# Kernel tuning notes

Measured on AMD Instinct MI355X. Metric: run time of the kernel, lower is better.

The kernel has to match this reference:

```python
import jax, jax.numpy as jnp
import numpy as np

B, U1, U2 = 4, 2048, 2048
C = 256      # in_feat_dim
F = 256      # feat_dim
M = 4        # num_modes
D = C // M   # attention_mode_dim = 64
ATTN_CLIP = 500.0
LN_EPS = 1e-12


def setup_inputs() -> dict:
    key = jax.random.key(0)
    ks = jax.random.split(key, 8)
    s = 0.02  # base_initializer_range
    inp = {
        "query_feat": jax.random.normal(ks[0], (B, U1, C), jnp.float32),
        "key_feat": jax.random.normal(ks[1], (B, U2, C), jnp.float32),
        "Wq": jax.random.normal(ks[2], (M * D, C), jnp.float32) * s,
        "bq": jnp.zeros((M * D,), jnp.float32),
    }
    # tie_qk_scheme='shared': key linear shares query weights
    inp["Wk"] = inp["Wq"]
    inp["bk"] = inp["bq"]
    inp["Wv"] = jax.random.normal(ks[3], (M * F, C), jnp.float32) * s  # first_linear, v_has_bias=False
    inp["W_mid"] = jax.random.normal(ks[4], (F, F), jnp.float32) * s   # MMSharedMid shared_linear
    inp["b_mid"] = jnp.zeros((F,), jnp.float32)
    inp["W_out"] = jax.random.normal(ks[5], (M, F, F), jnp.float32) * s  # grouped 1x1 conv, per mode
    inp["b_out"] = jnp.zeros((M, F), jnp.float32)
    inp["ln_g"] = jnp.ones((F,), jnp.float32)   # resout LayerNorm
    inp["ln_b"] = jnp.zeros((F,), jnp.float32)
    inp["W_score"] = jax.random.normal(ks[6], (1, F), jnp.float32) * s  # LearnedSoftAggregate
    inp["b_score"] = jnp.zeros((1,), jnp.float32)
    return inp


def _layer_norm(x, g, b):
    mu = jnp.mean(x, axis=-1, keepdims=True)
    var = jnp.var(x, axis=-1, keepdims=True)
    return (x - mu) * jax.lax.rsqrt(var + LN_EPS) * g + b


def reference(query_feat, key_feat, Wq, bq, Wk, bk, Wv, W_mid, b_mid,
              W_out, b_out, ln_g, ln_b, W_score, b_score):
    # --- tied-QK multi-mode attention ---
    q = (query_feat @ Wq.T + bq).reshape(B, U1, M, D)
    k = (key_feat @ Wk.T + bk).reshape(B, U2, M, D)
    scores = jnp.einsum('bimd,bjmd->bmij', q, k) / jnp.sqrt(jnp.float32(D))
    scores = jnp.clip(scores, -ATTN_CLIP, ATTN_CLIP)  # attn_clip
    probs = jax.nn.softmax(scores, axis=-1)           # [B, M, U1, U2]

    # --- ExpandedFeatTrans: value projection + fusion ---
    v = (key_feat @ Wv.T).reshape(B, U2, M, F)        # first_linear (no bias)
    fused = jnp.einsum('bmij,bjmf->bmif', probs, v)   # [B, M, U1, F]

    # MMSharedMid: shared linear over F + gelu (dropout = identity in eval)
    mid = jax.nn.gelu(fused @ W_mid.T + b_mid, approximate=False)

    # MMPrivateOutput: per-mode grouped 1x1 conv; NOTE the original code computes
    # x_comb = x + shortcut but then layer-norms x (shortcut dropped) - kept faithful.
    out = jnp.einsum('bmif,mgf->bmig', mid, W_out) + b_out[None, :, None, :]
    out = _layer_norm(out, ln_g, ln_b)                # [B, M, U1, F]

    # LearnedSoftAggregate over modes (group_dim=1, keepdim=False)
    mode_scores = out @ W_score.T + b_score           # [B, M, U1, 1]
    mode_probs = jax.nn.softmax(mode_scores, axis=1)
    return jnp.sum(out * mode_probs, axis=1)          # [B, U1, F]
```

## Files before the change

### kernel.cpp

```cpp
#include <hip/hip_runtime.h>

typedef __attribute__((ext_vector_type(8))) short short8;
typedef __attribute__((ext_vector_type(4))) float f32x4;
typedef __attribute__((ext_vector_type(16))) float f32x16;
typedef unsigned short u16t;
typedef unsigned int u32t;

#define MFMA16(a, b, c) __builtin_amdgcn_mfma_f32_16x16x32_bf16((a), (b), (c), 0, 0, 0)
#define MFMA32(a, b, c) __builtin_amdgcn_mfma_f32_32x32x16_bf16((a), (b), (c), 0, 0, 0)

__device__ __forceinline__ u16t f2bf(float f) {
  u32t u = __float_as_uint(f);
  u32t r = u + 0x7fffu + ((u >> 16) & 1u);
  return (u16t)(r >> 16);
}
__device__ __forceinline__ float bf2f(u16t b) {
  return __uint_as_float(((u32t)b) << 16);
}
__device__ __forceinline__ short8 pack8(float4 a0, float4 a1) {
  short8 r;
  r[0] = (short)f2bf(a0.x); r[1] = (short)f2bf(a0.y);
  r[2] = (short)f2bf(a0.z); r[3] = (short)f2bf(a0.w);
  r[4] = (short)f2bf(a1.x); r[5] = (short)f2bf(a1.y);
  r[6] = (short)f2bf(a1.z); r[7] = (short)f2bf(a1.w);
  return r;
}
__device__ __forceinline__ u32t packrhu(float a, float b) {
  u32t ua = __float_as_uint(a) + 0x8000u;
  u32t ub = __float_as_uint(b) + 0x8000u;
  return (ua >> 16) | (ub & 0xffff0000u);
}

__device__ __forceinline__ void proj_dev(
    const float* __restrict__ A, const float* __restrict__ W,
    const float* __restrict__ bias, float scale,
    u16t* __restrict__ out, int mode, int bx, int by,
    u16t* As, u16t* Ws) {
  const int tid = threadIdx.x;
  const int w = tid >> 6, lane = tid & 63, quad = lane >> 4, l15 = lane & 15;
  const int l31 = lane & 31, h8 = (lane >> 5) * 8;
  const int rt = bx * 64;
  const int ct = by * 64;
  const int wrow = (w >> 1) * 32, wcol = (w & 1) * 32;
  const int r2 = tid >> 3, c8 = tid & 7;

  const f32x4 fzero = {0.f, 0.f, 0.f, 0.f};
  f32x4 acc[2][2];
#pragma unroll
  for (int i = 0; i < 2; i++)
#pragma unroll
    for (int j = 0; j < 2; j++) acc[i][j] = fzero;

  for (int kt = 0; kt < 4; ++kt) {
    __syncthreads();
#pragma unroll
    for (int hh = 0; hh < 2; ++hh) {
      int rr = r2 + hh * 32;
      const float4* pa = (const float4*)(A + (size_t)(rt + rr) * 256 + kt * 64 + c8 * 8);
      const float4* pw = (const float4*)(W + (size_t)(ct + rr) * 256 + kt * 64 + c8 * 8);
      float4 w0 = pw[0], w1 = pw[1];
      w0.x *= scale; w0.y *= scale; w0.z *= scale; w0.w *= scale;
      w1.x *= scale; w1.y *= scale; w1.z *= scale; w1.w *= scale;
      *(short8*)&As[rr * 72 + c8 * 8] = pack8(pa[0], pa[1]);
      *(short8*)&Ws[rr * 72 + c8 * 8] = pack8(w0, w1);
    }
    __syncthreads();
#pragma unroll
    for (int ks = 0; ks < 2; ++ks) {
      short8 af0 = *(const short8*)&As[(wrow + l15) * 72 + ks * 32 + quad * 8];
      short8 af1 = *(const short8*)&As[(wrow + 16 + l15) * 72 + ks * 32 + quad * 8];
      short8 bw0 = *(const short8*)&Ws[(wcol + l15) * 72 + ks * 32 + quad * 8];
      short8 bw1 = *(const short8*)&Ws[(wcol + 16 + l15) * 72 + ks * 32 + quad * 8];
      acc[0][0] = MFMA16(af0, bw0, acc[0][0]);
      acc[0][1] = MFMA16(af0, bw1, acc[0][1]);
      acc[1][0] = MFMA16(af1, bw0, acc[1][0]);
      acc[1][1] = MFMA16(af1, bw1, acc[1][1]);
    }
  }

  __syncthreads();
  u16t* Cs = As;
  if (mode == 0) {
#pragma unroll
    for (int i = 0; i < 2; i++) {
      int rl = wrow + i * 16 + quad * 4;
#pragma unroll
      for (int j = 0; j < 2; j++) {
        int cl = wcol + j * 16 + l15;
        float bv = bias ? bias[ct + cl] * scale : 0.f;
#pragma unroll
        for (int rg = 0; rg < 4; ++rg)
          Cs[(rl + rg) * 72 + cl] = f2bf(acc[i][j][rg] + bv);
      }
    }
  } else {
#pragma unroll
    for (int i = 0; i < 2; i++) {
      int rl = wrow + i * 16 + quad * 4;
#pragma unroll
      for (int j = 0; j < 2; j++) {
        int cl = wcol + j * 16 + l15;
        ushort4 pk;
        pk.x = f2bf(acc[i][j][0]);
        pk.y = f2bf(acc[i][j][1]);
        pk.z = f2bf(acc[i][j][2]);
        pk.w = f2bf(acc[i][j][3]);
        *(ushort4*)&Cs[cl * 72 + rl] = pk;
      }
    }
  }
  __syncthreads();

#pragma unroll
  for (int t2 = 0; t2 < 2; ++t2) {
    short8 frag = *(const short8*)&Cs[(t2 * 32 + l31) * 72 + w * 16 + h8];
    size_t base;
    if (mode == 0) {
      int b = rt >> 11, m = by;
      int it32 = ((rt & 2047) >> 5) + t2;
      base = (((size_t)(b * 4 + m) * 64 + it32) * 4 + w) * 512;
    } else {
      int b = rt >> 11, m = by >> 2;
      int fb = ((by & 3) << 1) + t2;
      int jt16 = ((rt & 2047) >> 4) + w;
      base = (((size_t)(b * 4 + m) * 8 + fb) * 128 + jt16) * 512;
    }
    *(short8*)(out + base + lane * 8) = frag;
  }
}

__global__ __launch_bounds__(256) void prep_kernel(
    const float* __restrict__ query, const float* __restrict__ key,
    const float* __restrict__ Wq, const float* __restrict__ bq,
    const float* __restrict__ Wv, const float* __restrict__ Wm,
    const float* __restrict__ Wo,
    u16t* __restrict__ WmB, u16t* __restrict__ WoB,
    u16t* __restrict__ QfB, u16t* __restrict__ KfB, u16t* __restrict__ VfB) {
  __shared__ __align__(16) u16t As[64 * 72];
  __shared__ __align__(16) u16t Ws[64 * 72];
  const int blk = blockIdx.x;
  const int tid = threadIdx.x;
  if (blk < 256) {
    int i = blk * 256 + tid;
    WmB[i] = f2bf(Wm[i]);
    return;
  }
  if (blk < 1280) {
    int i = (blk - 256) * 256 + tid;
    WoB[i] = f2bf(Wo[i]);
    return;
  }
  const float *A, *W, *bias;
  float scale;
  u16t* out;
  int mode, local;
  if (blk < 1792) {
    local = blk - 1280; A = query; W = Wq; bias = bq; scale = 0.125f; out = QfB; mode = 0;
  } else if (blk < 2304) {
    local = blk - 1792; A = key; W = Wq; bias = bq; scale = 1.0f; out = KfB; mode = 0;
  } else {
    local = blk - 2304; A = key; W = Wv; bias = nullptr; scale = 1.0f; out = VfB; mode = 1;
  }
  proj_dev(A, W, bias, scale, out, mode, local & 127, local >> 7, As, Ws);
}

__global__ __launch_bounds__(512, 4) void attn_kernel(
    const u16t* __restrict__ Qf, const u16t* __restrict__ Kf,
    const u16t* __restrict__ Vf,
    const u16t* __restrict__ Wmid, const u16t* __restrict__ Wout,
    const float* __restrict__ b_mid, const float* __restrict__ b_out,
    const float* __restrict__ ln_g, const float* __restrict__ ln_b,
    const float* __restrict__ Wsc, const float* __restrict__ b_sc,
    u16t* __restrict__ out_ln, float* __restrict__ scoresWS) {
  __shared__ __align__(16) u16t smF[64 * 264];
  __shared__ __align__(16) u16t smP[2][64 * 132];
  __shared__ float smL[256];
  __shared__ float smR[256];
  __shared__ float smS[128];
  const int tid = threadIdx.x;
  const int w = tid >> 6, lane = tid & 63, quad = lane >> 4, l15 = lane & 15;
  const int l31 = lane & 31, h = lane >> 5;
  const int L = blockIdx.x;
  const int xcd = L & 7, slot = L >> 3;
  const int bm = xcd * 2 + (slot >> 5);
  const int it64 = slot & 31;
  const int m = bm & 3;
  const int q0 = it64 * 64;
  const int jw = w & 3, ihS = w >> 2;

  const size_t lane8 = (size_t)lane * 8;

  const u16t* qbase = Qf + ((size_t)(bm * 64 + it64 * 2 + ihS) * 4) * 512 + lane8;
  short8 qf4[4];
#pragma unroll
  for (int ksd = 0; ksd < 4; ++ksd)
    qf4[ksd] = *(const short8*)(qbase + ksd * 512);

  const u16t* kbase = Kf + ((size_t)bm * 256) * 512 + lane8;
  const u16t* vbase = Vf + ((size_t)(bm * 8 + w) * 128) * 512 + lane8;

  f32x16 facc[2];
#pragma unroll
  for (int j = 0; j < 2; j++)
#pragma unroll
    for (int r = 0; r < 16; r++) facc[j][r] = 0.f;
  float lsum = 0.f;

  short8 kf4[4];
#pragma unroll
  for (int ksd = 0; ksd < 4; ++ksd)
    kf4[ksd] = *(const short8*)(kbase + (size_t)jw * 2048 + ksd * 512);

  {
    f32x16 sacc;
#pragma unroll
    for (int r = 0; r < 16; r++) sacc[r] = 0.f;
#pragma unroll
    for (int ksd = 0; ksd < 4; ++ksd)
      sacc = MFMA32(kf4[ksd], qf4[ksd], sacc);
    float ls = 0.f;
#pragma unroll
    for (int tt = 0; tt < 8; ++tt) {
      const int jl = ((2 * tt) & 3) + 8 * ((2 * tt) >> 2) + 4 * h;
      float p0 = __expf(sacc[2 * tt]);
      float p1 = __expf(sacc[2 * tt + 1]);
      ls += p0 + p1;
      *(u32t*)&smP[0][(ihS * 32 + l31) * 132 + jw * 32 + jl] = packrhu(p0, p1);
    }
    lsum += ls;
  }
#pragma unroll
  for (int ksd = 0; ksd < 4; ++ksd)
    kf4[ksd] = *(const short8*)(kbase + (size_t)(4 + jw) * 2048 + ksd * 512);
  __syncthreads();

#pragma unroll 1
  for (int t = 0; t < 16; ++t) {
    u16t* Pb = &smP[t & 1][0];
    u16t* Pn = &smP[(t + 1) & 1][0];

    if (t < 15) {
      f32x16 sacc;
#pragma unroll
      for (int r = 0; r < 16; r++) sacc[r] = 0.f;
#pragma unroll
      for (int ksd = 0; ksd < 4; ++ksd)
        sacc = MFMA32(kf4[ksd], qf4[ksd], sacc);
      float ls = 0.f;
#pragma unroll
      for (int tt = 0; tt < 8; ++tt) {
        const int jl = ((2 * tt) & 3) + 8 * ((2 * tt) >> 2) + 4 * h;
        float p0 = __expf(sacc[2 * tt]);
        float p1 = __expf(sacc[2 * tt + 1]);
        ls += p0 + p1;
        *(u32t*)&Pn[(ihS * 32 + l31) * 132 + jw * 32 + jl] = packrhu(p0, p1);
      }
      lsum += ls;
    }
    if (t < 14) {
      const int jn = (t + 2) * 4 + jw;
#pragma unroll
      for (int ksd = 0; ksd < 4; ++ksd)
        kf4[ksd] = *(const short8*)(kbase + (size_t)jn * 2048 + ksd * 512);
    }
#pragma unroll
    for (int ks = 0; ks < 8; ++ks) {
      short8 vf = *(const short8*)(vbase + ((size_t)(t * 8 + ks)) * 512);
      short8 b0 = *(const short8*)&Pb[l31 * 132 + ks * 16 + h * 8];
      short8 b1 = *(const short8*)&Pb[(32 + l31) * 132 + ks * 16 + h * 8];
      facc[0] = MFMA32(vf, b0, facc[0]);
      facc[1] = MFMA32(vf, b1, facc[1]);
    }
    __syncthreads();
  }

  lsum += __shfl_xor(lsum, 32);
  if (h == 0) smL[w * 32 + l31] = lsum;
  __syncthreads();
  float inv[2];
#pragma unroll
  for (int ih = 0; ih < 2; ++ih)
    inv[ih] = 1.f / (smL[(ih * 4 + 0) * 32 + l31] + smL[(ih * 4 + 1) * 32 + l31] +
                     smL[(ih * 4 + 2) * 32 + l31] + smL[(ih * 4 + 3) * 32 + l31]);

#pragma unroll
  for (int ih = 0; ih < 2; ++ih) {
#pragma unroll
    for (int g = 0; g < 4; ++g) {
      int fbase = w * 32 + 8 * g + 4 * h;
      ushort4 pk4;
      pk4.x = f2bf(facc[ih][4 * g + 0] * inv[ih]);
      pk4.y = f2bf(facc[ih][4 * g + 1] * inv[ih]);
      pk4.z = f2bf(facc[ih][4 * g + 2] * inv[ih]);
      pk4.w = f2bf(facc[ih][4 * g + 3] * inv[ih]);
      *(ushort4*)&smF[(ih * 32 + l31) * 264 + fbase] = pk4;
    }
  }
  __syncthreads();

  const int rgrp = w >> 1, ch = w & 1;
  const int rowq = rgrp * 16 + quad * 4;
  const f32x4 fz4 = {0.f, 0.f, 0.f, 0.f};

  f32x4 macc[8];
#pragma unroll
  for (int i = 0; i < 8; i++) macc[i] = fz4;
  for (int kc = 0; kc < 8; ++kc) {
    short8 af = *(const short8*)&smF[(rgrp * 16 + l15) * 264 + kc * 32 + quad * 8];
#pragma unroll
    for (int nb = 0; nb < 8; ++nb) {
      short8 bw = *(const short8*)(Wmid + (size_t)(ch * 128 + nb * 16 + l15) * 256 + kc * 32 + quad * 8);
      macc[nb] = MFMA16(af, bw, macc[nb]);
    }
  }
#pragma unroll
  for (int nb = 0; nb < 8; ++nb) {
    int c = ch * 128 + nb * 16 + l15;
    float bmv = b_mid[c];
#pragma unroll
    for (int rg = 0; rg < 4; ++rg) {
      float x = macc[nb][rg] + bmv;
      macc[nb][rg] = 0.5f * x * (1.f + erff(x * 0.70710678118654752f));
    }
  }
  __syncthreads();
#pragma unroll
  for (int nb = 0; nb < 8; ++nb)
#pragma unroll
    for (int rg = 0; rg < 4; ++rg)
      smF[(rowq + rg) * 264 + ch * 128 + nb * 16 + l15] = f2bf(macc[nb][rg]);
  __syncthreads();

  const u16t* Wo = Wout + (size_t)m * 65536;
  f32x4 oacc[8];
#pragma unroll
  for (int i = 0; i < 8; i++) oacc[i] = fz4;
  for (int kc = 0; kc < 8; ++kc) {
    short8 af = *(const short8*)&smF[(rgrp * 16 + l15) * 264 + kc * 32 + quad * 8];
#pragma unroll
    for (int nb = 0; nb < 8; ++nb) {
      short8 bw = *(const short8*)(Wo + (size_t)(ch * 128 + nb * 16 + l15) * 256 + kc * 32 + quad * 8);
      oacc[nb] = MFMA16(af, bw, oacc[nb]);
    }
  }

  float sum[4] = {0, 0, 0, 0}, sq[4] = {0, 0, 0, 0};
#pragma unroll
  for (int nb = 0; nb < 8; ++nb) {
    int c = ch * 128 + nb * 16 + l15;
    float bo = b_out[m * 256 + c];
#pragma unroll
    for (int rg = 0; rg < 4; ++rg) {
      float x = oacc[nb][rg] + bo;
      oacc[nb][rg] = x;
      sum[rg] += x;
      sq[rg] += x * x;
    }
  }
#pragma unroll
  for (int rg = 0; rg < 4; ++rg) {
    float s = sum[rg], s2 = sq[rg];
    s += __shfl_xor(s, 1); s += __shfl_xor(s, 2); s += __shfl_xor(s, 4); s += __shfl_xor(s, 8);
    s2 += __shfl_xor(s2, 1); s2 += __shfl_xor(s2, 2); s2 += __shfl_xor(s2, 4); s2 += __shfl_xor(s2, 8);
    if (l15 == 0) {
      smR[(rowq + rg) + 64 * ch] = s;
      smR[128 + (rowq + rg) + 64 * ch] = s2;
    }
  }
  __syncthreads();
  float mu[4], rstd[4];
#pragma unroll
  for (int rg = 0; rg < 4; ++rg) {
    int r = rowq + rg;
    float s = smR[r] + smR[r + 64];
    float s2 = smR[128 + r] + smR[128 + r + 64];
    float mean = s * (1.f / 256.f);
    float var = s2 * (1.f / 256.f) - mean * mean;
    mu[rg] = mean;
    rstd[rg] = rsqrtf(var + 1e-12f);
  }

  float scp[4] = {0, 0, 0, 0};
#pragma unroll
  for (int nb = 0; nb < 8; ++nb) {
    int c = ch * 128 + nb * 16 + l15;
    float g = ln_g[c], bb2 = ln_b[c], wsv = Wsc[c];
#pragma unroll
    for (int rg = 0; rg < 4; ++rg) {
      float xn = (oacc[nb][rg] - mu[rg]) * rstd[rg] * g + bb2;
      out_ln[((size_t)bm * 2048 + (q0 + rowq + rg)) * 256 + c] = f2bf(xn);
      scp[rg] += xn * wsv;
    }
  }
#pragma unroll
  for (int rg = 0; rg < 4; ++rg) {
    float s = scp[rg];
    s += __shfl_xor(s, 1); s += __shfl_xor(s, 2); s += __shfl_xor(s, 4); s += __shfl_xor(s, 8);
    if (l15 == 0) smS[(rowq + rg) + 64 * ch] = s;
  }
  __syncthreads();
  if (ch == 0 && l15 == 0) {
#pragma unroll
    for (int rg = 0; rg < 4; ++rg) {
      int r = rowq + rg;
      scoresWS[bm * 2048 + q0 + r] = smS[r] + smS[r + 64] + b_sc[0];
    }
  }
}

__global__ __launch_bounds__(256) void agg_kernel(
    const u16t* __restrict__ out_ln, const float* __restrict__ scoresWS,
    float* __restrict__ out) {
  const int row = blockIdx.x;
  const int c = threadIdx.x;
  const int b = row >> 11, i = row & 2047;
  float s0 = scoresWS[(b * 4 + 0) * 2048 + i];
  float s1 = scoresWS[(b * 4 + 1) * 2048 + i];
  float s2 = scoresWS[(b * 4 + 2) * 2048 + i];
  float s3 = scoresWS[(b * 4 + 3) * 2048 + i];
  float mx = fmaxf(fmaxf(s0, s1), fmaxf(s2, s3));
  float e0 = __expf(s0 - mx), e1 = __expf(s1 - mx), e2 = __expf(s2 - mx), e3 = __expf(s3 - mx);
  float inv = 1.f / (e0 + e1 + e2 + e3);
  float acc = e0 * inv * bf2f(out_ln[((size_t)(b * 4 + 0) * 2048 + i) * 256 + c]) +
              e1 * inv * bf2f(out_ln[((size_t)(b * 4 + 1) * 2048 + i) * 256 + c]) +
              e2 * inv * bf2f(out_ln[((size_t)(b * 4 + 2) * 2048 + i) * 256 + c]) +
              e3 * inv * bf2f(out_ln[((size_t)(b * 4 + 3) * 2048 + i) * 256 + c]);
  out[(size_t)row * 256 + c] = acc;
}

extern "C" void kernel_launch(void* const* d_in, const int* in_sizes, int n_in,
                              void* d_out, int out_size, void* d_ws, size_t ws_size,
                              hipStream_t stream) {
  (void)in_sizes; (void)n_in; (void)out_size; (void)ws_size;
  const float* query = (const float*)d_in[0];
  const float* key   = (const float*)d_in[1];
  const float* Wq    = (const float*)d_in[2];
  const float* bq    = (const float*)d_in[3];
  const float* Wv    = (const float*)d_in[6];
  const float* Wm    = (const float*)d_in[7];
  const float* bmid  = (const float*)d_in[8];
  const float* Wo    = (const float*)d_in[9];
  const float* bo    = (const float*)d_in[10];
  const float* lng   = (const float*)d_in[11];
  const float* lnb   = (const float*)d_in[12];
  const float* Wsc   = (const float*)d_in[13];
  const float* bsc   = (const float*)d_in[14];

  char* p = (char*)d_ws;
  u16t* QfB = (u16t*)p; p += (size_t)2097152 * 2;
  u16t* KfB = (u16t*)p; p += (size_t)2097152 * 2;
  u16t* VfB = (u16t*)p; p += (size_t)8388608 * 2;
  u16t* WmB = (u16t*)p; p += (size_t)65536 * 2;
  u16t* WoB = (u16t*)p; p += (size_t)262144 * 2;
  u16t* outLn = (u16t*)p; p += (size_t)8388608 * 2;
  float* scWS = (float*)p; p += (size_t)32768 * 4;

  prep_kernel<<<4352, 256, 0, stream>>>(query, key, Wq, bq, Wv, Wm, Wo,
                                        WmB, WoB, QfB, KfB, VfB);

  attn_kernel<<<512, 512, 0, stream>>>(QfB, KfB, VfB, WmB, WoB,
                                       bmid, bo, lng, lnb, Wsc, bsc,
                                       outLn, scWS);

  agg_kernel<<<8192, 256, 0, stream>>>(outLn, scWS, (float*)d_out);
}
```

Before: 281.8 us.

## Halve attention query tile to 32 rows, doubling blocks and occupancy

Each attention block now handles 32 query rows instead of 64. All 8 waves split the key dimension (8 key tiles per step, 8 steps) and each holds one accumulator. The probability buffer and the fused-feature buffer share one LDS allocation, launch bounds ask for 8 blocks per CU, and the grid doubles to 1024 blocks. This should raise occupancy and cut the tail effect, at the cost of reading each V and K tile twice as often in total and paying more per-block overhead in the MLP/LN epilogue.

```diff
diff --git a/kernel.cpp b/kernel.cpp
--- a/kernel.cpp
+++ b/kernel.cpp
@@ -164,7 +164,7 @@
   proj_dev(A, W, bias, scale, out, mode, local & 127, local >> 7, As, Ws);
 }
 
-__global__ __launch_bounds__(512, 4) void attn_kernel(
+__global__ __launch_bounds__(512, 8) void attn_kernel(
     const u16t* __restrict__ Qf, const u16t* __restrict__ Kf,
     const u16t* __restrict__ Vf,
     const u16t* __restrict__ Wmid, const u16t* __restrict__ Wout,
@@ -172,8 +172,7 @@
     const float* __restrict__ ln_g, const float* __restrict__ ln_b,
     const float* __restrict__ Wsc, const float* __restrict__ b_sc,
     u16t* __restrict__ out_ln, float* __restrict__ scoresWS) {
-  __shared__ __align__(16) u16t smF[64 * 264];
-  __shared__ __align__(16) u16t smP[2][64 * 132];
+  __shared__ __align__(16) u16t smU[16640];
   __shared__ float smL[256];
   __shared__ float smR[256];
   __shared__ float smS[128];
@@ -182,15 +181,14 @@
   const int l31 = lane & 31, h = lane >> 5;
   const int L = blockIdx.x;
   const int xcd = L & 7, slot = L >> 3;
-  const int bm = xcd * 2 + (slot >> 5);
-  const int it64 = slot & 31;
+  const int bm = xcd * 2 + (slot >> 6);
+  const int it32 = slot & 63;
   const int m = bm & 3;
-  const int q0 = it64 * 64;
-  const int jw = w & 3, ihS = w >> 2;
+  const int q0 = it32 * 32;
 
   const size_t lane8 = (size_t)lane * 8;
 
-  const u16t* qbase = Qf + ((size_t)(bm * 64 + it64 * 2 + ihS) * 4) * 512 + lane8;
+  const u16t* qbase = Qf + ((size_t)(bm * 64 + it32) * 4) * 512 + lane8;
   short8 qf4[4];
 #pragma unroll
   for (int ksd = 0; ksd < 4; ++ksd)
@@ -199,17 +197,15 @@
   const u16t* kbase = Kf + ((size_t)bm * 256) * 512 + lane8;
   const u16t* vbase = Vf + ((size_t)(bm * 8 + w) * 128) * 512 + lane8;
 
-  f32x16 facc[2];
-#pragma unroll
-  for (int j = 0; j < 2; j++)
-#pragma unroll
-    for (int r = 0; r < 16; r++) facc[j][r] = 0.f;
+  f32x16 facc;
+#pragma unroll
+  for (int r = 0; r < 16; r++) facc[r] = 0.f;
   float lsum = 0.f;
 
   short8 kf4[4];
 #pragma unroll
   for (int ksd = 0; ksd < 4; ++ksd)
-    kf4[ksd] = *(const short8*)(kbase + (size_t)jw * 2048 + ksd * 512);
+    kf4[ksd] = *(const short8*)(kbase + (size_t)w * 2048 + ksd * 512);
 
   {
     f32x16 sacc;
@@ -225,21 +221,21 @@
       float p0 = __expf(sacc[2 * tt]);
       float p1 = __expf(sacc[2 * tt + 1]);
       ls += p0 + p1;
-      *(u32t*)&smP[0][(ihS * 32 + l31) * 132 + jw * 32 + jl] = packrhu(p0, p1);
+      *(u32t*)&smU[l31 * 260 + w * 32 + jl] = packrhu(p0, p1);
     }
     lsum += ls;
   }
 #pragma unroll
   for (int ksd = 0; ksd < 4; ++ksd)
-    kf4[ksd] = *(const short8*)(kbase + (size_t)(4 + jw) * 2048 + ksd * 512);
+    kf4[ksd] = *(const short8*)(kbase + (size_t)(8 + w) * 2048 + ksd * 512);
   __syncthreads();
 
 #pragma unroll 1
-  for (int t = 0; t < 16; ++t) {
-    u16t* Pb = &smP[t & 1][0];
-    u16t* Pn = &smP[(t + 1) & 1][0];
-
-    if (t < 15) {
+  for (int t = 0; t < 8; ++t) {
+    u16t* Pb = (t & 1) ? smU + 8320 : smU;
+    u16t* Pn = (t & 1) ? smU : smU + 8320;
+
+    if (t < 7) {
       f32x16 sacc;
 #pragma unroll
       for (int r = 0; r < 16; r++) sacc[r] = 0.f;
@@ -253,23 +249,21 @@
         float p0 = __expf(sacc[2 * tt]);
         float p1 = __expf(sacc[2 * tt + 1]);
         ls += p0 + p1;
-        *(u32t*)&Pn[(ihS * 32 + l31) * 132 + jw * 32 + jl] = packrhu(p0, p1);
+        *(u32t*)&Pn[l31 * 260 + w * 32 + jl] = packrhu(p0, p1);
       }
       lsum += ls;
     }
-    if (t < 14) {
-      const int jn = (t + 2) * 4 + jw;
+    if (t < 6) {
+      const int jn = (t + 2) * 8 + w;
 #pragma unroll
       for (int ksd = 0; ksd < 4; ++ksd)
         kf4[ksd] = *(const short8*)(kbase + (size_t)jn * 2048 + ksd * 512);
     }
 #pragma unroll
-    for (int ks = 0; ks < 8; ++ks) {
-      short8 vf = *(const short8*)(vbase + ((size_t)(t * 8 + ks)) * 512);
-      short8 b0 = *(const short8*)&Pb[l31 * 132 + ks * 16 + h * 8];
-      short8 b1 = *(const short8*)&Pb[(32 + l31) * 132 + ks * 16 + h * 8];
-      facc[0] = MFMA32(vf, b0, facc[0]);
-      facc[1] = MFMA32(vf, b1, facc[1]);
+    for (int ks = 0; ks < 16; ++ks) {
+      short8 vf = *(const short8*)(vbase + ((size_t)(t * 16 + ks)) * 512);
+      short8 bb = *(const short8*)&Pb[l31 * 260 + ks * 16 + h * 8];
+      facc = MFMA32(vf, bb, facc);
     }
     __syncthreads();
   }
@@ -277,45 +271,45 @@
   lsum += __shfl_xor(lsum, 32);
   if (h == 0) smL[w * 32 + l31] = lsum;
   __syncthreads();
-  float inv[2];
-#pragma unroll
-  for (int ih = 0; ih < 2; ++ih)
-    inv[ih] = 1.f / (smL[(ih * 4 + 0) * 32 + l31] + smL[(ih * 4 + 1) * 32 + l31] +
-                     smL[(ih * 4 + 2) * 32 + l31] + smL[(ih * 4 + 3) * 32 + l31]);
-
-#pragma unroll
-  for (int ih = 0; ih < 2; ++ih) {
-#pragma unroll
-    for (int g = 0; g < 4; ++g) {
-      int fbase = w * 32 + 8 * g + 4 * h;
-      ushort4 pk4;
-      pk4.x = f2bf(facc[ih][4 * g + 0] * inv[ih]);
-      pk4.y = f2bf(facc[ih][4 * g + 1] * inv[ih]);
-      pk4.z = f2bf(facc[ih][4 * g + 2] * inv[ih]);
-      pk4.w = f2bf(facc[ih][4 * g + 3] * inv[ih]);
-      *(ushort4*)&smF[(ih * 32 + l31) * 264 + fbase] = pk4;
-    }
-  }
-  __syncthreads();
-
-  const int rgrp = w >> 1, ch = w & 1;
+  float inv;
+  {
+    float s = 0.f;
+#pragma unroll
+    for (int q = 0; q < 8; ++q) s += smL[q * 32 + l31];
+    inv = 1.f / s;
+  }
+
+  u16t* const smF = smU;
+#pragma unroll
+  for (int g = 0; g < 4; ++g) {
+    int fbase = w * 32 + 8 * g + 4 * h;
+    ushort4 pk4;
+    pk4.x = f2bf(facc[4 * g + 0] * inv);
+    pk4.y = f2bf(facc[4 * g + 1] * inv);
+    pk4.z = f2bf(facc[4 * g + 2] * inv);
+    pk4.w = f2bf(facc[4 * g + 3] * inv);
+    *(ushort4*)&smF[l31 * 264 + fbase] = pk4;
+  }
+  __syncthreads();
+
+  const int rgrp = w >> 2, cq = w & 3;
   const int rowq = rgrp * 16 + quad * 4;
   const f32x4 fz4 = {0.f, 0.f, 0.f, 0.f};
 
-  f32x4 macc[8];
-#pragma unroll
-  for (int i = 0; i < 8; i++) macc[i] = fz4;
+  f32x4 macc[4];
+#pragma unroll
+  for (int i = 0; i < 4; i++) macc[i] = fz4;
   for (int kc = 0; kc < 8; ++kc) {
     short8 af = *(const short8*)&smF[(rgrp * 16 + l15) * 264 + kc * 32 + quad * 8];
 #pragma unroll
-    for (int nb = 0; nb < 8; ++nb) {
-      short8 bw = *(const short8*)(Wmid + (size_t)(ch * 128 + nb * 16 + l15) * 256 + kc * 32 + quad * 8);
+    for (int nb = 0; nb < 4; ++nb) {
+      short8 bw = *(const short8*)(Wmid + (size_t)(cq * 64 + nb * 16 + l15) * 256 + kc * 32 + quad * 8);
       macc[nb] = MFMA16(af, bw, macc[nb]);
     }
   }
 #pragma unroll
-  for (int nb = 0; nb < 8; ++nb) {
-    int c = ch * 128 + nb * 16 + l15;
+  for (int nb = 0; nb < 4; ++nb) {
+    int c = cq * 64 + nb * 16 + l15;
     float bmv = b_mid[c];
 #pragma unroll
     for (int rg = 0; rg < 4; ++rg) {
@@ -325,29 +319,29 @@
   }
   __syncthreads();
 #pragma unroll
-  for (int nb = 0; nb < 8; ++nb)
+  for (int nb = 0; nb < 4; ++nb)
 #pragma unroll
     for (int rg = 0; rg < 4; ++rg)
-      smF[(rowq + rg) * 264 + ch * 128 + nb * 16 + l15] = f2bf(macc[nb][rg]);
+      smF[(rowq + rg) * 264 + cq * 64 + nb * 16 + l15] = f2bf(macc[nb][rg]);
   __syncthreads();
 
   const u16t* Wo = Wout + (size_t)m * 65536;
-  f32x4 oacc[8];
-#pragma unroll
-  for (int i = 0; i < 8; i++) oacc[i] = fz4;
+  f32x4 oacc[4];
+#pragma unroll
+  for (int i = 0; i < 4; i++) oacc[i] = fz4;
   for (int kc = 0; kc < 8; ++kc) {
     short8 af = *(const short8*)&smF[(rgrp * 16 + l15) * 264 + kc * 32 + quad * 8];
 #pragma unroll
-    for (int nb = 0; nb < 8; ++nb) {
-      short8 bw = *(const short8*)(Wo + (size_t)(ch * 128 + nb * 16 + l15) * 256 + kc * 32 + quad * 8);
+    for (int nb = 0; nb < 4; ++nb) {
+      short8 bw = *(const short8*)(Wo + (size_t)(cq * 64 + nb * 16 + l15) * 256 + kc * 32 + quad * 8);
       oacc[nb] = MFMA16(af, bw, oacc[nb]);
     }
   }
 
   float sum[4] = {0, 0, 0, 0}, sq[4] = {0, 0, 0, 0};
 #pragma unroll
-  for (int nb = 0; nb < 8; ++nb) {
-    int c = ch * 128 + nb * 16 + l15;
+  for (int nb = 0; nb < 4; ++nb) {
+    int c = cq * 64 + nb * 16 + l15;
     float bo = b_out[m * 256 + c];
 #pragma unroll
     for (int rg = 0; rg < 4; ++rg) {
@@ -363,8 +357,8 @@
     s += __shfl_xor(s, 1); s += __shfl_xor(s, 2); s += __shfl_xor(s, 4); s += __shfl_xor(s, 8);
     s2 += __shfl_xor(s2, 1); s2 += __shfl_xor(s2, 2); s2 += __shfl_xor(s2, 4); s2 += __shfl_xor(s2, 8);
     if (l15 == 0) {
-      smR[(rowq + rg) + 64 * ch] = s;
-      smR[128 + (rowq + rg) + 64 * ch] = s2;
+      smR[(rowq + rg) + 32 * cq] = s;
+      smR[128 + (rowq + rg) + 32 * cq] = s2;
     }
   }
   __syncthreads();
@@ -372,8 +366,8 @@
 #pragma unroll
   for (int rg = 0; rg < 4; ++rg) {
     int r = rowq + rg;
-    float s = smR[r] + smR[r + 64];
-    float s2 = smR[128 + r] + smR[128 + r + 64];
+    float s = smR[r] + smR[r + 32] + smR[r + 64] + smR[r + 96];
+    float s2 = smR[128 + r] + smR[128 + r + 32] + smR[128 + r + 64] + smR[128 + r + 96];
     float mean = s * (1.f / 256.f);
     float var = s2 * (1.f / 256.f) - mean * mean;
     mu[rg] = mean;
@@ -382,8 +376,8 @@
 
   float scp[4] = {0, 0, 0, 0};
 #pragma unroll
-  for (int nb = 0; nb < 8; ++nb) {
-    int c = ch * 128 + nb * 16 + l15;
+  for (int nb = 0; nb < 4; ++nb) {
+    int c = cq * 64 + nb * 16 + l15;
     float g = ln_g[c], bb2 = ln_b[c], wsv = Wsc[c];
 #pragma unroll
     for (int rg = 0; rg < 4; ++rg) {
@@ -396,14 +390,15 @@
   for (int rg = 0; rg < 4; ++rg) {
     float s = scp[rg];
     s += __shfl_xor(s, 1); s += __shfl_xor(s, 2); s += __shfl_xor(s, 4); s += __shfl_xor(s, 8);
-    if (l15 == 0) smS[(rowq + rg) + 64 * ch] = s;
-  }
-  __syncthreads();
-  if (ch == 0 && l15 == 0) {
+    if (l15 == 0) smS[(rowq + rg) + 32 * cq] = s;
+  }
+  __syncthreads();
+  if (cq == 0 && l15 == 0) {
 #pragma unroll
     for (int rg = 0; rg < 4; ++rg) {
       int r = rowq + rg;
-      scoresWS[bm * 2048 + q0 + r] = smS[r] + smS[r + 64] + b_sc[0];
+      scoresWS[bm * 2048 + q0 + r] =
+          smS[r] + smS[r + 32] + smS[r + 64] + smS[r + 96] + b_sc[0];
     }
   }
 }
@@ -458,9 +453,9 @@
   prep_kernel<<<4352, 256, 0, stream>>>(query, key, Wq, bq, Wv, Wm, Wo,
                                         WmB, WoB, QfB, KfB, VfB);
 
-  attn_kernel<<<512, 512, 0, stream>>>(QfB, KfB, VfB, WmB, WoB,
-                                       bmid, bo, lng, lnb, Wsc, bsc,
-                                       outLn, scWS);
+  attn_kernel<<<1024, 512, 0, stream>>>(QfB, KfB, VfB, WmB, WoB,
+                                        bmid, bo, lng, lnb, Wsc, bsc,
+                                        outLn, scWS);
 
   agg_kernel<<<8192, 256, 0, stream>>>(outLn, scWS, (float*)d_out);
 }
```

Measured after the change: 309.6 us. +9.9%, slower.
